# Kernel optimization log

Measured on AMD Instinct MI355X. Metric: run time of the kernel, lower is better.

## Reference

```python
import jax, jax.numpy as jnp
import numpy as np
from jax import lax

E, BANDS, T, NCLS, TOPK, DBN = 62, 5, 64, 4, 10, 32
NODE_DIM = 512  # 128 channels * 4 width after conv-pool chain


def _conv(x, w, b):
    # x: (N,C,H,W), w: (O,I,kh,kw) torch layout
    y = lax.conv_general_dilated(x, w, window_strides=(1, 1), padding='VALID',
                                 dimension_numbers=('NCHW', 'OIHW', 'NCHW'))
    return y + b[None, :, None, None]


def _maxpool_1x2(x):
    return lax.reduce_window(x, -jnp.inf, lax.max, (1, 1, 1, 2), (1, 1, 1, 2), 'VALID')


def _sogc(H, W_bn, gc_w, gc_b, k):
    # H: (B,E,Din). Dropout omitted (eval mode).
    G = jnp.tanh(jnp.einsum('bed,kd->bek', H, W_bn))            # (B,E,DBN)
    A = jax.nn.softmax(jnp.einsum('bek,bfk->bef', G, G), axis=-1)  # (B,E,E)
    vals, idxs = lax.top_k(A, k)                                  # (B,E,k)
    B = H.shape[0]
    bi = jnp.arange(B)[:, None, None]
    ei = jnp.arange(H.shape[1])[None, :, None]
    A_sparse = jnp.zeros_like(A).at[bi, ei, idxs].set(vals)
    M = jnp.einsum('bef,bfd->bed', A_sparse, H)                   # (B,E,Din)
    return jax.nn.relu(jnp.einsum('bed,od->beo', M, gc_w) + gc_b)


def setup_inputs() -> dict:
    key = jax.random.key(0)
    ks = jax.random.split(key, 20)
    r = lambda i, shape, s: (jax.random.normal(ks[i], shape, dtype=jnp.float32) * s)
    B = 512
    return {
        'x': r(0, (B, E, BANDS, T), 1.0),
        'conv1_w': r(1, (32, 1, 5, 5), 0.2), 'conv1_b': r(2, (32,), 0.02),
        'conv2_w': r(3, (64, 32, 1, 5), 0.08), 'conv2_b': r(4, (64,), 0.02),
        'conv3_w': r(5, (128, 64, 1, 5), 0.06), 'conv3_b': r(6, (128,), 0.02),
        'Wbn1': r(7, (DBN, NODE_DIM), 0.04),
        'gc1_w': r(8, (64, NODE_DIM), 0.04), 'gc1_b': r(9, (64,), 0.02),
        'Wbn2': r(10, (DBN, 64), 0.12),
        'gc2_w': r(11, (64, 64), 0.12), 'gc2_b': r(12, (64,), 0.02),
        'Wbn3': r(13, (DBN, 64), 0.12),
        'gc3_w': r(14, (64, 64), 0.12), 'gc3_b': r(15, (64,), 0.02),
        'cls_w': r(16, (NCLS, E * 64), 0.02), 'cls_b': r(17, (NCLS,), 0.02),
    }


def reference(x, conv1_w, conv1_b, conv2_w, conv2_b, conv3_w, conv3_b,
              Wbn1, gc1_w, gc1_b, Wbn2, gc2_w, gc2_b, Wbn3, gc3_w, gc3_b,
              cls_w, cls_b):
    B = x.shape[0]
    h = x.reshape(B * E, 1, BANDS, T)
    h = _maxpool_1x2(jax.nn.relu(_conv(h, conv1_w, conv1_b)))  # (BE,32,1,30)
    h = _maxpool_1x2(jax.nn.relu(_conv(h, conv2_w, conv2_b)))  # (BE,64,1,13)
    h = _maxpool_1x2(jax.nn.relu(_conv(h, conv3_w, conv3_b)))  # (BE,128,1,4)
    h = h.reshape(B, E, NODE_DIM)
    h = _sogc(h, Wbn1, gc1_w, gc1_b, TOPK)
    h = _sogc(h, Wbn2, gc2_w, gc2_b, TOPK)
    h = _sogc(h, Wbn3, gc3_w, gc3_b, TOPK)
    logits = h.reshape(B, E * 64) @ cls_w.T + cls_b
    return logits
```

## Files before the change

kernel.cpp:

```cpp
#include <hip/hip_runtime.h>

#define E_NODES 62
#define TOPK 10

__global__ __launch_bounds__(256) void wt_kernel(
    const float* __restrict__ w2, const float* __restrict__ w3,
    const float* __restrict__ Wbn1, const float* __restrict__ gc1w,
    float* __restrict__ w2t, float* __restrict__ w3t, float* __restrict__ wt)
{
  const int j = blockIdx.x * 256 + threadIdx.x;
  if (j < 10240) {
    const int r = j >> 6, o = j & 63;
    w2t[j] = w2[o * 160 + r];
  } else if (j < 51200) {
    const int k = j - 10240;
    const int r = k >> 7, o = k & 127;
    w3t[k] = w3[o * 320 + r];
  } else {
    const int k = j - 51200;
    const int d4 = k / 384, rem = k - d4 * 384;
    const int jj = rem >> 2, q = rem & 3;
    const int d = d4 * 4 + q;
    wt[k] = (jj < 32) ? Wbn1[jj * 512 + d] : gc1w[(jj - 32) * 512 + d];
  }
}

__device__ __forceinline__ void stage16(const float* __restrict__ g,
                                        float* l, int n4, int tid) {
  for (int i = tid; i < n4; i += 256)
    __builtin_amdgcn_global_load_lds(
        (const __attribute__((address_space(1))) void*)(g + 4 * i),
        (__attribute__((address_space(3))) void*)(l + 4 * i), 16, 0, 0);
}


__global__ __launch_bounds__(256, 3) void conv_chain_kernel(
    const float* __restrict__ x,
    const float* __restrict__ w1, const float* __restrict__ b1,
    const float* __restrict__ w2t, const float* __restrict__ b2,
    const float* __restrict__ w3t, const float* __restrict__ b3,
    const float* __restrict__ WT, float* __restrict__ GP)
{
  __shared__ float sm[13312];
  float* s_h1  = sm;
  float* s_h2  = sm + 4096;
  float* s_wa  = sm + 8192;
  float* s_wb  = sm + 10752;
  float* s_w1  = sm + 8192;
  float* s_img = sm + 9024;

  const int tid = threadIdx.x;
  const int n0 = blockIdx.x * 4;
  const int im = tid >> 6;
  const int lane = tid & 63;

  stage16(x + (size_t)n0 * 320, s_img, 320, tid);
  for (int i = tid; i < 832; i += 256) s_w1[i] = (i < 800) ? w1[i] : b1[i - 800];
  __syncthreads();

  stage16(w2t, s_wb, 640, tid);

  {
    const int tp = lane & 31;
    const int half = lane >> 5;
    if (tp < 30) {
      const float* ib = s_img + im * 320;
      const int t0 = 2 * tp;
      float r[5][6];
#pragma unroll
      for (int kr = 0; kr < 5; ++kr)
#pragma unroll
        for (int c = 0; c < 6; ++c) r[kr][c] = ib[kr * 64 + t0 + c];
#pragma unroll 4
      for (int oi = 0; oi < 16; ++oi) {
        const int o = half * 16 + oi;
        const float* w = s_w1 + o * 25;
        float s0 = s_w1[800 + o], s1 = s0;
#pragma unroll
        for (int kr = 0; kr < 5; ++kr) {
#pragma unroll
          for (int k = 0; k < 5; ++k) {
            const float wv = w[kr * 5 + k];
            s0 += r[kr][k] * wv;
            s1 += r[kr][k + 1] * wv;
          }
        }
        s_h1[im * 1024 + o * 32 + tp] = fmaxf(fmaxf(s0, s1), 0.f);
      }
    }
  }
  __syncthreads();

  {
    const int o = lane;
    const float bia = b2[o];

    {
      float acc0[7], acc1[7];
#pragma unroll
      for (int t = 0; t < 7; ++t) { acc0[t] = bia; acc1[t] = bia; }
#pragma unroll 1
      for (int c = 0; c < 4; ++c) {
        const float* rb = (c & 1) ? s_wa : s_wb;
        float*       nb = (c & 1) ? s_wb : s_wa;
        stage16(w2t + ((c < 3) ? (c + 1) * 2560 : 0), nb, 640, tid);
#pragma unroll 4
        for (int cl = 0; cl < 8; ++cl) {
          const float* hr = s_h1 + im * 1024 + (c * 8 + cl) * 32;
          float r[18];
#pragma unroll
          for (int q = 0; q < 4; ++q) {
            const float4 v = *(const float4*)(hr + q * 4);
            r[q * 4] = v.x; r[q * 4 + 1] = v.y; r[q * 4 + 2] = v.z; r[q * 4 + 3] = v.w;
          }
          { const float2 v = *(const float2*)(hr + 16); r[16] = v.x; r[17] = v.y; }
          const float* wb = rb + cl * 320 + o;
#pragma unroll
          for (int k = 0; k < 5; ++k) {
            const float wv = wb[k * 64];
#pragma unroll
            for (int t = 0; t < 7; ++t) {
              acc0[t] += r[2 * t + k] * wv;
              acc1[t] += r[2 * t + 1 + k] * wv;
            }
          }
        }
        __syncthreads();
      }
#pragma unroll
      for (int t = 0; t < 7; ++t)
        s_h2[im * 1024 + o * 16 + t] = fmaxf(fmaxf(acc0[t], acc1[t]), 0.f);
    }

    {
      float acc0[6], acc1[6];
#pragma unroll
      for (int t = 0; t < 6; ++t) { acc0[t] = bia; acc1[t] = bia; }
#pragma unroll 1
      for (int c = 0; c < 4; ++c) {
        const float* rb = (c & 1) ? s_wa : s_wb;
        float*       nb = (c & 1) ? s_wb : s_wa;
        stage16((c < 3) ? (w2t + (c + 1) * 2560) : w3t, nb, 640, tid);
#pragma unroll 4
        for (int cl = 0; cl < 8; ++cl) {
          const float* hr = s_h1 + im * 1024 + (c * 8 + cl) * 32;
          float r[18];
#pragma unroll
          for (int q = 0; q < 4; ++q) {
            const float4 v = *(const float4*)(hr + 12 + q * 4);
            r[q * 4] = v.x; r[q * 4 + 1] = v.y; r[q * 4 + 2] = v.z; r[q * 4 + 3] = v.w;
          }
          { const float2 v = *(const float2*)(hr + 28); r[16] = v.x; r[17] = v.y; }
          const float* wb = rb + cl * 320 + o;
#pragma unroll
          for (int k = 0; k < 5; ++k) {
            const float wv = wb[k * 64];
#pragma unroll
            for (int t = 0; t < 6; ++t) {
              const int t0 = 2 * t + 2;
              acc0[t] += r[t0 + k] * wv;
              acc1[t] += r[t0 + 1 + k] * wv;
            }
          }
        }
        __syncthreads();
      }
#pragma unroll
      for (int t = 0; t < 6; ++t)
        s_h2[im * 1024 + o * 16 + 7 + t] = fmaxf(fmaxf(acc0[t], acc1[t]), 0.f);
    }
  }

  stage16(WT, s_h1, 768, tid);

  {
    const int oc = lane;
    float acc[2][8];
#pragma unroll
    for (int t = 0; t < 8; ++t) {
      acc[0][t] = b3[oc];
      acc[1][t] = b3[64 + oc];
    }
#pragma unroll 1
    for (int k = 0; k < 16; ++k) {
      const float* rb = (k & 1) ? s_wa : s_wb;
      float*       nb = (k & 1) ? s_wb : s_wa;
      if (k < 15) stage16(w3t + (k + 1) * 2560, nb, 640, tid);
#pragma unroll 2
      for (int cl = 0; cl < 4; ++cl) {
        const float* hr = s_h2 + im * 1024 + (k * 4 + cl) * 16;
        float r[12];
#pragma unroll
        for (int q = 0; q < 3; ++q) {
          const float4 v = *(const float4*)(hr + q * 4);
          r[q * 4] = v.x; r[q * 4 + 1] = v.y; r[q * 4 + 2] = v.z; r[q * 4 + 3] = v.w;
        }
        const float* wb = rb + cl * 640 + oc;
#pragma unroll
        for (int kk = 0; kk < 5; ++kk) {
          const float wv0 = wb[kk * 128];
          const float wv1 = wb[kk * 128 + 64];
#pragma unroll
          for (int t = 0; t < 8; ++t) {
            acc[0][t] += r[t + kk] * wv0;
            acc[1][t] += r[t + kk] * wv1;
          }
        }
      }
      __syncthreads();
    }
    float* h3w = s_wb + im * 520;
    float4 ov;
    ov.x = fmaxf(fmaxf(acc[0][0], acc[0][1]), 0.f);
    ov.y = fmaxf(fmaxf(acc[0][2], acc[0][3]), 0.f);
    ov.z = fmaxf(fmaxf(acc[0][4], acc[0][5]), 0.f);
    ov.w = fmaxf(fmaxf(acc[0][6], acc[0][7]), 0.f);
    *(float4*)(h3w + oc * 4) = ov;
    ov.x = fmaxf(fmaxf(acc[1][0], acc[1][1]), 0.f);
    ov.y = fmaxf(fmaxf(acc[1][2], acc[1][3]), 0.f);
    ov.z = fmaxf(fmaxf(acc[1][4], acc[1][5]), 0.f);
    ov.w = fmaxf(fmaxf(acc[1][6], acc[1][7]), 0.f);
    *(float4*)(h3w + 256 + oc * 4) = ov;
  }

  {
    stage16(WT + 3072, s_h2, 768, tid);
    __syncthreads();
    const float* h3 = s_wb + im * 520;
    const int jP = 32 + lane, jG = lane & 31;
    float accp = 0.f, accg = 0.f;
#pragma unroll 1
    for (int s = 0; s < 16; ++s) {
      const float* z = (s & 1) ? s_h2 : s_h1;
#pragma unroll
      for (int d4 = 0; d4 < 8; ++d4) {
        const float4 hv = *(const float4*)(h3 + s * 32 + d4 * 4);
        const float4 wp = *(const float4*)(z + d4 * 384 + jP * 4);
        const float4 wg = *(const float4*)(z + d4 * 384 + jG * 4);
        accp += hv.x * wp.x + hv.y * wp.y + hv.z * wp.z + hv.w * wp.w;
        accg += hv.x * wg.x + hv.y * wg.y + hv.z * wg.z + hv.w * wg.w;
      }
      __syncthreads();
      if (s < 14) stage16(WT + (s + 2) * 3072, (s & 1) ? s_h2 : s_h1, 768, tid);
    }
    float* gpo = GP + (size_t)(n0 + im) * 96;
    gpo[32 + lane] = accp;
    if (lane < 32) gpo[lane] = 1.f - 2.f / (__expf(2.f * accg) + 1.f);
  }
}

__global__ __launch_bounds__(256) void sogc1_kernel(
    const float* __restrict__ GP, const float* __restrict__ gcb,
    float* __restrict__ Hout)
{
  __shared__ float sG[62 * 33];
  __shared__ float sP[62 * 64];
  __shared__ float stv[620];
  __shared__ int   sti[620];
  const int b = blockIdx.x, tid = threadIdx.x;
  const int lane = tid & 63, wave = tid >> 6;

  const float* gp = GP + (size_t)b * 62 * 96;
  for (int i = tid; i < 62 * 96; i += 256) {
    const int e = i / 96, q = i - e * 96;
    const float v = gp[i];
    if (q < 32) sG[e * 33 + q] = v; else sP[e * 64 + (q - 32)] = v;
  }
  __syncthreads();

  for (int e = wave; e < E_NODES; e += 4) {
    float sc = -1e30f;
    if (lane < E_NODES) {
      float s = 0.f;
#pragma unroll
      for (int k = 0; k < 32; ++k) s += sG[e * 33 + k] * sG[lane * 33 + k];
      sc = s;
    }
    float mx = sc;
#pragma unroll
    for (int off = 32; off; off >>= 1) mx = fmaxf(mx, __shfl_xor(mx, off));
    float p = (lane < E_NODES) ? __expf(sc - mx) : 0.f;
    float sum = p;
#pragma unroll
    for (int off = 32; off; off >>= 1) sum += __shfl_xor(sum, off);
    p = p / sum;
    float v = (lane < E_NODES) ? p : -1.f;
#pragma unroll 1
    for (int it = 0; it < TOPK; ++it) {
      float bv = v; int bi = lane;
#pragma unroll
      for (int off = 32; off; off >>= 1) {
        const float ov = __shfl_xor(bv, off);
        const int   oi = __shfl_xor(bi, off);
        if (ov > bv || (ov == bv && oi < bi)) { bv = ov; bi = oi; }
      }
      if (lane == 0) { stv[e * 10 + it] = bv; sti[e * 10 + it] = bi; }
      if (lane == bi) v = -1.f;
    }
  }
  __syncthreads();

  for (int e = wave; e < E_NODES; e += 4) {
    float acc = gcb[lane];
#pragma unroll
    for (int j = 0; j < TOPK; ++j)
      acc += stv[e * 10 + j] * sP[sti[e * 10 + j] * 64 + lane];
    Hout[((size_t)b * E_NODES + e) * 64 + lane] = fmaxf(acc, 0.f);
  }
}

template <bool CLS>
__global__ __launch_bounds__(256) void sogc64_kernel(
    const float* __restrict__ Hin, const float* __restrict__ Wbn,
    const float* __restrict__ gcw, const float* __restrict__ gcb,
    const float* __restrict__ cw, const float* __restrict__ cb,
    float* __restrict__ outbuf)
{
  extern __shared__ float sm[];
  float* sH  = sm;
  float* sWt = sm + 4030;
  float* sG  = sm + 10238;
  float* sP  = sm + 12284;
  float* stv = sm + 16252;
  int*   sti = (int*)(sm + 16872);
  float* sred = sm + 17492;

  const int b = blockIdx.x, tid = threadIdx.x;
  const int lane = tid & 63, wave = tid >> 6;

  const float* Hb = Hin + (size_t)b * 62 * 64;
  for (int i = tid; i < 62 * 64; i += 256)
    sH[(i >> 6) * 65 + (i & 63)] = Hb[i];
  for (int i = tid; i < 64 * 64; i += 256)
    sWt[(i & 63) * 97 + (i >> 6)] = gcw[i];
  for (int i = tid; i < 32 * 64; i += 256)
    sWt[(i & 63) * 97 + 64 + (i >> 6)] = Wbn[i];
  __syncthreads();

  for (int e = wave; e < E_NODES; e += 4) {
    const float* hrow = sH + e * 65;
    const float* wp = sWt + lane;
    const float* wg = sWt + 64 + (lane & 31);
    float accp = 0.f, accg = 0.f;
#pragma unroll 8
    for (int d = 0; d < 64; ++d) {
      const float h = hrow[d];
      accp += h * wp[d * 97];
      accg += h * wg[d * 97];
    }
    sP[e * 64 + lane] = accp;
    if (lane < 32) sG[e * 33 + lane] = 1.f - 2.f / (__expf(2.f * accg) + 1.f);
  }
  __syncthreads();

  for (int e = wave; e < E_NODES; e += 4) {
    float sc = -1e30f;
    if (lane < E_NODES) {
      float s = 0.f;
#pragma unroll
      for (int k = 0; k < 32; ++k) s += sG[e * 33 + k] * sG[lane * 33 + k];
      sc = s;
    }
    float mx = sc;
#pragma unroll
    for (int off = 32; off; off >>= 1) mx = fmaxf(mx, __shfl_xor(mx, off));
    float p = (lane < E_NODES) ? __expf(sc - mx) : 0.f;
    float sum = p;
#pragma unroll
    for (int off = 32; off; off >>= 1) sum += __shfl_xor(sum, off);
    p = p / sum;
    float v = (lane < E_NODES) ? p : -1.f;
#pragma unroll 1
    for (int it = 0; it < TOPK; ++it) {
      float bv = v; int bi = lane;
#pragma unroll
      for (int off = 32; off; off >>= 1) {
        const float ov = __shfl_xor(bv, off);
        const int   oi = __shfl_xor(bi, off);
        if (ov > bv || (ov == bv && oi < bi)) { bv = ov; bi = oi; }
      }
      if (lane == 0) { stv[e * 10 + it] = bv; sti[e * 10 + it] = bi; }
      if (lane == bi) v = -1.f;
    }
  }
  __syncthreads();

  float accn[4] = {0.f, 0.f, 0.f, 0.f};
  for (int e = wave; e < E_NODES; e += 4) {
    float acc = gcb[lane];
#pragma unroll
    for (int j = 0; j < TOPK; ++j)
      acc += stv[e * 10 + j] * sP[sti[e * 10 + j] * 64 + lane];
    acc = fmaxf(acc, 0.f);
    if (CLS) {
#pragma unroll
      for (int n = 0; n < 4; ++n)
        accn[n] += acc * cw[n * 3968 + e * 64 + lane];
    } else {
      outbuf[((size_t)b * E_NODES + e) * 64 + lane] = acc;
    }
  }
  if (CLS) {
#pragma unroll
    for (int n = 0; n < 4; ++n) {
      float s = accn[n];
#pragma unroll
      for (int off = 32; off; off >>= 1) s += __shfl_xor(s, off);
      if (lane == 0) sred[wave * 4 + n] = s;
    }
    __syncthreads();
    if (tid < 4)
      outbuf[b * 4 + tid] = cb[tid] + sred[tid] + sred[4 + tid] + sred[8 + tid] + sred[12 + tid];
  }
}

extern "C" void kernel_launch(void* const* d_in, const int* in_sizes, int n_in,
                              void* d_out, int out_size, void* d_ws, size_t ws_size,
                              hipStream_t stream) {
  const float* x    = (const float*)d_in[0];
  const float* c1w  = (const float*)d_in[1];
  const float* c1b  = (const float*)d_in[2];
  const float* c2w  = (const float*)d_in[3];
  const float* c2b  = (const float*)d_in[4];
  const float* c3w  = (const float*)d_in[5];
  const float* c3b  = (const float*)d_in[6];
  const float* Wbn1 = (const float*)d_in[7];
  const float* gc1w = (const float*)d_in[8];
  const float* gc1b = (const float*)d_in[9];
  const float* Wbn2 = (const float*)d_in[10];
  const float* gc2w = (const float*)d_in[11];
  const float* gc2b = (const float*)d_in[12];
  const float* Wbn3 = (const float*)d_in[13];
  const float* gc3w = (const float*)d_in[14];
  const float* gc3b = (const float*)d_in[15];
  const float* clsw = (const float*)d_in[16];
  const float* clsb = (const float*)d_in[17];
  float* out = (float*)d_out;

  float* wsf = (float*)d_ws;
  float* W2T = wsf;
  float* W3T = wsf + 10240;
  float* WT  = wsf + 51200;
  float* GP  = wsf + 100352;
  float* Hs1 = GP + (size_t)3047424;
  float* Hs2 = Hs1 + (size_t)2031616;

  const int SOGC64_BYTES = 17508 * 4;

  (void)hipFuncSetAttribute((const void*)sogc64_kernel<false>,
                            hipFuncAttributeMaxDynamicSharedMemorySize, SOGC64_BYTES);
  (void)hipFuncSetAttribute((const void*)sogc64_kernel<true>,
                            hipFuncAttributeMaxDynamicSharedMemorySize, SOGC64_BYTES);

  wt_kernel<<<392, 256, 0, stream>>>(c2w, c3w, Wbn1, gc1w, W2T, W3T, WT);
  conv_chain_kernel<<<7936, 256, 0, stream>>>(x, c1w, c1b, W2T, c2b, W3T, c3b,
                                              WT, GP);
  sogc1_kernel<<<512, 256, 0, stream>>>(GP, gc1b, Hs1);
  sogc64_kernel<false><<<512, 256, SOGC64_BYTES, stream>>>(
      Hs1, Wbn2, gc2w, gc2b, nullptr, nullptr, Hs2);
  sogc64_kernel<true><<<512, 256, SOGC64_BYTES, stream>>>(
      Hs2, Wbn3, gc3w, gc3b, clsw, clsb, out);
}
```

Measured before the change: 1.167 ms.

## Fuse three SOGC graph-conv layers and classifier into one per-batch kernel

Replaces the separate sogc1 kernel and the two sogc64 launches with a single kernel that keeps node features in shared memory across all three graph-conv layers and the classifier. This removes two kernel launches and the global round trips of the intermediate Hs1/Hs2 buffers. Layer-3 weight loading is overlapped with the layer-2 top-k phase. The cost is a single long-running kernel with 512 blocks that uses the larger shared-memory footprint for every stage.

```diff
diff --git a/kernel.cpp b/kernel.cpp
--- a/kernel.cpp
+++ b/kernel.cpp
@@ -33,7 +33,6 @@
         (__attribute__((address_space(3))) void*)(l + 4 * i), 16, 0, 0);
 }
 
-
 __global__ __launch_bounds__(256, 3) void conv_chain_kernel(
     const float* __restrict__ x,
     const float* __restrict__ w1, const float* __restrict__ b1,
@@ -249,72 +248,14 @@
   }
 }
 
-__global__ __launch_bounds__(256) void sogc1_kernel(
-    const float* __restrict__ GP, const float* __restrict__ gcb,
-    float* __restrict__ Hout)
-{
-  __shared__ float sG[62 * 33];
-  __shared__ float sP[62 * 64];
-  __shared__ float stv[620];
-  __shared__ int   sti[620];
-  const int b = blockIdx.x, tid = threadIdx.x;
-  const int lane = tid & 63, wave = tid >> 6;
-
-  const float* gp = GP + (size_t)b * 62 * 96;
-  for (int i = tid; i < 62 * 96; i += 256) {
-    const int e = i / 96, q = i - e * 96;
-    const float v = gp[i];
-    if (q < 32) sG[e * 33 + q] = v; else sP[e * 64 + (q - 32)] = v;
-  }
-  __syncthreads();
-
-  for (int e = wave; e < E_NODES; e += 4) {
-    float sc = -1e30f;
-    if (lane < E_NODES) {
-      float s = 0.f;
-#pragma unroll
-      for (int k = 0; k < 32; ++k) s += sG[e * 33 + k] * sG[lane * 33 + k];
-      sc = s;
-    }
-    float mx = sc;
-#pragma unroll
-    for (int off = 32; off; off >>= 1) mx = fmaxf(mx, __shfl_xor(mx, off));
-    float p = (lane < E_NODES) ? __expf(sc - mx) : 0.f;
-    float sum = p;
-#pragma unroll
-    for (int off = 32; off; off >>= 1) sum += __shfl_xor(sum, off);
-    p = p / sum;
-    float v = (lane < E_NODES) ? p : -1.f;
-#pragma unroll 1
-    for (int it = 0; it < TOPK; ++it) {
-      float bv = v; int bi = lane;
-#pragma unroll
-      for (int off = 32; off; off >>= 1) {
-        const float ov = __shfl_xor(bv, off);
-        const int   oi = __shfl_xor(bi, off);
-        if (ov > bv || (ov == bv && oi < bi)) { bv = ov; bi = oi; }
-      }
-      if (lane == 0) { stv[e * 10 + it] = bv; sti[e * 10 + it] = bi; }
-      if (lane == bi) v = -1.f;
-    }
-  }
-  __syncthreads();
-
-  for (int e = wave; e < E_NODES; e += 4) {
-    float acc = gcb[lane];
-#pragma unroll
-    for (int j = 0; j < TOPK; ++j)
-      acc += stv[e * 10 + j] * sP[sti[e * 10 + j] * 64 + lane];
-    Hout[((size_t)b * E_NODES + e) * 64 + lane] = fmaxf(acc, 0.f);
-  }
-}
-
-template <bool CLS>
-__global__ __launch_bounds__(256) void sogc64_kernel(
-    const float* __restrict__ Hin, const float* __restrict__ Wbn,
-    const float* __restrict__ gcw, const float* __restrict__ gcb,
-    const float* __restrict__ cw, const float* __restrict__ cb,
-    float* __restrict__ outbuf)
+__global__ __launch_bounds__(256) void sogc_fused_kernel(
+    const float* __restrict__ GP,   const float* __restrict__ gc1b,
+    const float* __restrict__ Wbn2, const float* __restrict__ gc2w,
+    const float* __restrict__ gc2b,
+    const float* __restrict__ Wbn3, const float* __restrict__ gc3w,
+    const float* __restrict__ gc3b,
+    const float* __restrict__ cw,   const float* __restrict__ cb,
+    float* __restrict__ out)
 {
   extern __shared__ float sm[];
   float* sH  = sm;
@@ -328,79 +269,110 @@
   const int b = blockIdx.x, tid = threadIdx.x;
   const int lane = tid & 63, wave = tid >> 6;
 
-  const float* Hb = Hin + (size_t)b * 62 * 64;
-  for (int i = tid; i < 62 * 64; i += 256)
-    sH[(i >> 6) * 65 + (i & 63)] = Hb[i];
+  const float* gp = GP + (size_t)b * 62 * 96;
+  for (int i = tid; i < 62 * 96; i += 256) {
+    const int e = i / 96, q = i - e * 96;
+    const float v = gp[i];
+    if (q < 32) sG[e * 33 + q] = v; else sP[e * 64 + (q - 32)] = v;
+  }
   for (int i = tid; i < 64 * 64; i += 256)
-    sWt[(i & 63) * 97 + (i >> 6)] = gcw[i];
+    sWt[(i & 63) * 97 + (i >> 6)] = gc2w[i];
   for (int i = tid; i < 32 * 64; i += 256)
-    sWt[(i & 63) * 97 + 64 + (i >> 6)] = Wbn[i];
-  __syncthreads();
-
+    sWt[(i & 63) * 97 + 64 + (i >> 6)] = Wbn2[i];
+  __syncthreads();
+
+#define TOPK_PHASE()                                                          \
+  for (int e = wave; e < E_NODES; e += 4) {                                   \
+    float sc = -1e30f;                                                        \
+    if (lane < E_NODES) {                                                     \
+      float s = 0.f;                                                          \
+      _Pragma("unroll")                                                       \
+      for (int k = 0; k < 32; ++k) s += sG[e * 33 + k] * sG[lane * 33 + k];   \
+      sc = s;                                                                 \
+    }                                                                         \
+    float mx = sc;                                                            \
+    _Pragma("unroll")                                                         \
+    for (int off = 32; off; off >>= 1) mx = fmaxf(mx, __shfl_xor(mx, off));   \
+    float p = (lane < E_NODES) ? __expf(sc - mx) : 0.f;                       \
+    float sum = p;                                                            \
+    _Pragma("unroll")                                                         \
+    for (int off = 32; off; off >>= 1) sum += __shfl_xor(sum, off);           \
+    p = p / sum;                                                              \
+    float v = (lane < E_NODES) ? p : -1.f;                                    \
+    _Pragma("unroll 1")                                                       \
+    for (int it = 0; it < TOPK; ++it) {                                       \
+      float bv = v; int bi = lane;                                            \
+      _Pragma("unroll")                                                       \
+      for (int off = 32; off; off >>= 1) {                                    \
+        const float ov = __shfl_xor(bv, off);                                 \
+        const int   oi = __shfl_xor(bi, off);                                 \
+        if (ov > bv || (ov == bv && oi < bi)) { bv = ov; bi = oi; }           \
+      }                                                                       \
+      if (lane == 0) { stv[e * 10 + it] = bv; sti[e * 10 + it] = bi; }        \
+      if (lane == bi) v = -1.f;                                               \
+    }                                                                         \
+  }
+
+#define GP_PHASE()                                                            \
+  for (int e = wave; e < E_NODES; e += 4) {                                   \
+    const float* hrow = sH + e * 65;                                          \
+    const float* wp = sWt + lane;                                             \
+    const float* wg = sWt + 64 + (lane & 31);                                 \
+    float accp = 0.f, accg = 0.f;                                             \
+    _Pragma("unroll 8")                                                       \
+    for (int d = 0; d < 64; ++d) {                                            \
+      const float h = hrow[d];                                                \
+      accp += h * wp[d * 97];                                                 \
+      accg += h * wg[d * 97];                                                 \
+    }                                                                         \
+    sP[e * 64 + lane] = accp;                                                 \
+    if (lane < 32) sG[e * 33 + lane] = 1.f - 2.f / (__expf(2.f * accg) + 1.f);\
+  }
+
+  TOPK_PHASE();
+  __syncthreads();
   for (int e = wave; e < E_NODES; e += 4) {
-    const float* hrow = sH + e * 65;
-    const float* wp = sWt + lane;
-    const float* wg = sWt + 64 + (lane & 31);
-    float accp = 0.f, accg = 0.f;
-#pragma unroll 8
-    for (int d = 0; d < 64; ++d) {
-      const float h = hrow[d];
-      accp += h * wp[d * 97];
-      accg += h * wg[d * 97];
-    }
-    sP[e * 64 + lane] = accp;
-    if (lane < 32) sG[e * 33 + lane] = 1.f - 2.f / (__expf(2.f * accg) + 1.f);
-  }
-  __syncthreads();
-
-  for (int e = wave; e < E_NODES; e += 4) {
-    float sc = -1e30f;
-    if (lane < E_NODES) {
-      float s = 0.f;
-#pragma unroll
-      for (int k = 0; k < 32; ++k) s += sG[e * 33 + k] * sG[lane * 33 + k];
-      sc = s;
-    }
-    float mx = sc;
-#pragma unroll
-    for (int off = 32; off; off >>= 1) mx = fmaxf(mx, __shfl_xor(mx, off));
-    float p = (lane < E_NODES) ? __expf(sc - mx) : 0.f;
-    float sum = p;
-#pragma unroll
-    for (int off = 32; off; off >>= 1) sum += __shfl_xor(sum, off);
-    p = p / sum;
-    float v = (lane < E_NODES) ? p : -1.f;
-#pragma unroll 1
-    for (int it = 0; it < TOPK; ++it) {
-      float bv = v; int bi = lane;
-#pragma unroll
-      for (int off = 32; off; off >>= 1) {
-        const float ov = __shfl_xor(bv, off);
-        const int   oi = __shfl_xor(bi, off);
-        if (ov > bv || (ov == bv && oi < bi)) { bv = ov; bi = oi; }
-      }
-      if (lane == 0) { stv[e * 10 + it] = bv; sti[e * 10 + it] = bi; }
-      if (lane == bi) v = -1.f;
-    }
-  }
-  __syncthreads();
-
-  float accn[4] = {0.f, 0.f, 0.f, 0.f};
-  for (int e = wave; e < E_NODES; e += 4) {
-    float acc = gcb[lane];
+    float acc = gc1b[lane];
 #pragma unroll
     for (int j = 0; j < TOPK; ++j)
       acc += stv[e * 10 + j] * sP[sti[e * 10 + j] * 64 + lane];
-    acc = fmaxf(acc, 0.f);
-    if (CLS) {
+    sH[e * 65 + lane] = fmaxf(acc, 0.f);
+  }
+  __syncthreads();
+
+  GP_PHASE();
+  __syncthreads();
+  for (int i = tid; i < 64 * 64; i += 256)
+    sWt[(i & 63) * 97 + (i >> 6)] = gc3w[i];
+  for (int i = tid; i < 32 * 64; i += 256)
+    sWt[(i & 63) * 97 + 64 + (i >> 6)] = Wbn3[i];
+  TOPK_PHASE();
+  __syncthreads();
+  for (int e = wave; e < E_NODES; e += 4) {
+    float acc = gc2b[lane];
+#pragma unroll
+    for (int j = 0; j < TOPK; ++j)
+      acc += stv[e * 10 + j] * sP[sti[e * 10 + j] * 64 + lane];
+    sH[e * 65 + lane] = fmaxf(acc, 0.f);
+  }
+  __syncthreads();
+
+  GP_PHASE();
+  __syncthreads();
+  TOPK_PHASE();
+  __syncthreads();
+  {
+    float accn[4] = {0.f, 0.f, 0.f, 0.f};
+    for (int e = wave; e < E_NODES; e += 4) {
+      float acc = gc3b[lane];
+#pragma unroll
+      for (int j = 0; j < TOPK; ++j)
+        acc += stv[e * 10 + j] * sP[sti[e * 10 + j] * 64 + lane];
+      acc = fmaxf(acc, 0.f);
 #pragma unroll
       for (int n = 0; n < 4; ++n)
         accn[n] += acc * cw[n * 3968 + e * 64 + lane];
-    } else {
-      outbuf[((size_t)b * E_NODES + e) * 64 + lane] = acc;
-    }
-  }
-  if (CLS) {
+    }
 #pragma unroll
     for (int n = 0; n < 4; ++n) {
       float s = accn[n];
@@ -410,8 +382,10 @@
     }
     __syncthreads();
     if (tid < 4)
-      outbuf[b * 4 + tid] = cb[tid] + sred[tid] + sred[4 + tid] + sred[8 + tid] + sred[12 + tid];
-  }
+      out[b * 4 + tid] = cb[tid] + sred[tid] + sred[4 + tid] + sred[8 + tid] + sred[12 + tid];
+  }
+#undef TOPK_PHASE
+#undef GP_PHASE
 }
 
 extern "C" void kernel_launch(void* const* d_in, const int* in_sizes, int n_in,
@@ -442,22 +416,15 @@
   float* W3T = wsf + 10240;
   float* WT  = wsf + 51200;
   float* GP  = wsf + 100352;
-  float* Hs1 = GP + (size_t)3047424;
-  float* Hs2 = Hs1 + (size_t)2031616;
-
-  const int SOGC64_BYTES = 17508 * 4;
-
-  (void)hipFuncSetAttribute((const void*)sogc64_kernel<false>,
-                            hipFuncAttributeMaxDynamicSharedMemorySize, SOGC64_BYTES);
-  (void)hipFuncSetAttribute((const void*)sogc64_kernel<true>,
-                            hipFuncAttributeMaxDynamicSharedMemorySize, SOGC64_BYTES);
+
+  const int SOGC_BYTES = 17508 * 4;
+
+  (void)hipFuncSetAttribute((const void*)sogc_fused_kernel,
+                            hipFuncAttributeMaxDynamicSharedMemorySize, SOGC_BYTES);
 
   wt_kernel<<<392, 256, 0, stream>>>(c2w, c3w, Wbn1, gc1w, W2T, W3T, WT);
   conv_chain_kernel<<<7936, 256, 0, stream>>>(x, c1w, c1b, W2T, c2b, W3T, c3b,
                                               WT, GP);
-  sogc1_kernel<<<512, 256, 0, stream>>>(GP, gc1b, Hs1);
-  sogc64_kernel<false><<<512, 256, SOGC64_BYTES, stream>>>(
-      Hs1, Wbn2, gc2w, gc2b, nullptr, nullptr, Hs2);
-  sogc64_kernel<true><<<512, 256, SOGC64_BYTES, stream>>>(
-      Hs2, Wbn3, gc3w, gc3b, clsw, clsb, out);
+  sogc_fused_kernel<<<512, 256, SOGC_BYTES, stream>>>(
+      GP, gc1b, Wbn2, gc2w, gc2b, Wbn3, gc3w, gc3b, clsw, clsb, out);
 }
```

Measured after the change: 1.147 ms. Within noise of the previous version (-1.7%).
